# Optimization experiments

Hardware: AMD Instinct MI355X
Metric: run time of the kernel (lower is better)

## Reference

```python
import jax, jax.numpy as jnp
import numpy as np
from jax.scipy.special import logsumexp

NUM_TAGS = 128
B, S = 256, 1024


def setup_inputs() -> dict:
    key = jax.random.key(0)
    k1, k2, k3, k4, k5 = jax.random.split(key, 5)
    emissions = jax.random.normal(k1, (B, S, NUM_TAGS), dtype=jnp.float32)
    masks = jnp.ones((B, S), dtype=jnp.float32)
    tags = jax.random.randint(k2, (B, S), 0, NUM_TAGS, dtype=jnp.int64)
    transitions = jax.random.normal(k3, (NUM_TAGS, NUM_TAGS), dtype=jnp.float32)
    start_transitions = jax.random.normal(k4, (NUM_TAGS,), dtype=jnp.float32)
    end_transitions = jax.random.normal(k5, (NUM_TAGS,), dtype=jnp.float32)
    return {"emissions": emissions, "masks": masks, "tags": tags,
            "transitions": transitions, "start_transitions": start_transitions,
            "end_transitions": end_transitions}


def _crf_loss(emissions, masks, tags, transitions, start_transitions, end_transitions):
    b, s, t = emissions.shape

    # ---- forward algorithm (log partition) ----
    def step(alpha, xs):
        emit, m = xs  # emit: (B,T), m: (B,)
        # next[b,j] = logsumexp_i(alpha[b,i] + trans[i,j] + emit[b,j])
        nxt = logsumexp(alpha[:, :, None] + transitions[None, :, :] + emit[:, None, :], axis=1)
        alpha = jnp.where(m[:, None] > 0, nxt, alpha)
        return alpha, None

    alpha0 = jnp.broadcast_to(start_transitions[None, :], (b, t))
    # note: original torch code includes i=0 in the recurrence (applies transitions
    # from start_transitions into the first emission) -- replicated faithfully.
    alpha, _ = jax.lax.scan(step, alpha0,
                            (jnp.swapaxes(emissions, 0, 1), masks.T))
    log_z = logsumexp(alpha + end_transitions[None, :], axis=1)  # (B,)

    # ---- gold sequence score (vectorized over time) ----
    bidx = jnp.arange(b)
    score = start_transitions[tags[:, 0]]
    emit_g = jnp.take_along_axis(emissions, tags[:, :, None], axis=2)[..., 0]  # (B,S)
    score = score + jnp.sum(emit_g[:, : s - 1] * masks[:, : s - 1], axis=1)
    trans_g = transitions[tags[:, : s - 1], tags[:, 1:]]  # (B,S-1)
    score = score + jnp.sum(trans_g * masks[:, 1:], axis=1)
    last_ix = jnp.maximum(jnp.sum(masks, axis=1) - 1.0, 0.0).astype(jnp.int32)
    score = score + emissions[bidx, last_ix, tags[:, -1]] * masks[:, -1]
    score = score + end_transitions[tags[:, -1]] * masks[:, -1]

    return jnp.mean(log_z - score)


def reference(emissions, masks, tags, transitions, start_transitions, end_transitions):
    return _crf_loss(emissions, masks, tags, transitions, start_transitions, end_transitions)
```

## Files before the change

kernel.cpp:

```cpp
#include <hip/hip_runtime.h>

#define NT 128
#define SEQ 1024
#define NB 256

typedef _Float16 half2v __attribute__((ext_vector_type(2)));

#define DPP_MAX_STEP(x, ctrl)                                                   \
    fmaxf((x), __builtin_bit_cast(float, __builtin_amdgcn_update_dpp(           \
        __builtin_bit_cast(int, (x)), __builtin_bit_cast(int, (x)),             \
        (ctrl), 0xf, 0xf, false)))

__device__ __forceinline__ float wave_max_dpp(float x) {
    x = DPP_MAX_STEP(x, 0x111);
    x = DPP_MAX_STEP(x, 0x112);
    x = DPP_MAX_STEP(x, 0x114);
    x = DPP_MAX_STEP(x, 0x118);
    x = DPP_MAX_STEP(x, 0x142);
    x = DPP_MAX_STEP(x, 0x143);
    return __builtin_bit_cast(float, __builtin_amdgcn_readlane(
        __builtin_bit_cast(int, x), 63));
}

#define CRF_STEP(RC, RN, MC, DO_PRE, K)                                          \
    {                                                                            \
        float mcur = MC;                                                         \
        if (DO_PRE) {                                                            \
            RC = *(const float2*)(emp + (K) * NT);                               \
            MC = mpp[K];                                                         \
        }                                                                        \
        float A[4] = {0.f, 0.f, 0.f, 0.f};                                       \
        float B[4] = {0.f, 0.f, 0.f, 0.f};                                       \
        _Pragma("unroll")                                                        \
        for (int j = 0; j < 64; ++j) {                                           \
            half2v p = __builtin_bit_cast(half2v,                                \
                __builtin_amdgcn_readlane((int)pk, j));                          \
            A[j & 3] = __builtin_amdgcn_fdot2(p, E0[j], A[j & 3], false);        \
            B[j & 3] = __builtin_amdgcn_fdot2(p, E1[j], B[j & 3], false);        \
        }                                                                        \
        float v0 = ((A[0] + A[1]) + (A[2] + A[3])) * ex.x;                       \
        float v1 = ((B[0] + B[1]) + (B[2] + B[3])) * ex.y;                       \
        if (mcur > 0.0f) { cur0 = v0; cur1 = v1; offset += offadd; }             \
        pk = __builtin_bit_cast(unsigned int,                                    \
                                __builtin_amdgcn_cvt_pkrtz(cur0, cur1));         \
        mx  = wave_max_dpp(fmaxf(cur0, cur1));                                   \
        inv = __builtin_amdgcn_rcpf(256.0f * mx);                                \
        offadd = __logf(mx) + 5.545177444479562f;                                \
        ex.x = __expf(RN.x) * inv;                                               \
        ex.y = __expf(RN.y) * inv;                                               \
    }

__global__ __launch_bounds__(64, 1) void crf_scan_kernel(
    const float* __restrict__ emissions,
    const float* __restrict__ masks,
    const int*   __restrict__ tags,
    const float* __restrict__ transitions,
    const float* __restrict__ start_t,
    const float* __restrict__ end_t,
    float* __restrict__ out_per_batch)
{
    const int b  = blockIdx.x;
    const int l  = threadIdx.x;
    const int c0 = 2 * l;
    const int c1 = 2 * l + 1;

    __shared__ float msk_s[SEQ];

    half2v E0[64], E1[64];
    #pragma unroll
    for (int r = 0; r < 64; ++r) {
        float2 ta = *(const float2*)&transitions[(2 * r)     * NT + c0];
        float2 tb = *(const float2*)&transitions[(2 * r + 1) * NT + c0];
        E0[r] = half2v{(_Float16)__expf(ta.x), (_Float16)__expf(tb.x)};
        E1[r] = half2v{(_Float16)__expf(ta.y), (_Float16)__expf(tb.y)};
    }

    for (int s = l; s < SEQ; s += 64)
        msk_s[s] = masks[b * SEQ + s];

    float cur0 = __expf(start_t[c0]);
    float cur1 = __expf(start_t[c1]);
    unsigned int pk = __builtin_bit_cast(unsigned int,
                                        __builtin_amdgcn_cvt_pkrtz(cur0, cur1));
    float offset = 0.0f;

    float mx  = wave_max_dpp(fmaxf(cur0, cur1));
    float inv = __builtin_amdgcn_rcpf(256.0f * mx);
    float offadd = __logf(mx) + 5.545177444479562f;

    const float* eb  = emissions + (size_t)b * SEQ * NT;
    const float* mkp = masks + b * SEQ;

    float2 ring0 = *(const float2*)&eb[(size_t)0 * NT + c0];
    float2 ring1 = *(const float2*)&eb[(size_t)1 * NT + c0];
    float2 ring2 = *(const float2*)&eb[(size_t)2 * NT + c0];
    float2 ring3 = *(const float2*)&eb[(size_t)3 * NT + c0];
    float  mr0 = mkp[0], mr1 = mkp[1], mr2 = mkp[2], mr3 = mkp[3];

    float2 ex;
    ex.x = __expf(ring0.x) * inv;
    ex.y = __expf(ring0.y) * inv;

    const float* emp = eb + 4 * NT + c0;
    const float* mpp = mkp + 4;

    for (int it = 0; it < (SEQ - 4) / 4; ++it) {
        CRF_STEP(ring0, ring1, mr0, true, 0)
        CRF_STEP(ring1, ring2, mr1, true, 1)
        CRF_STEP(ring2, ring3, mr2, true, 2)
        CRF_STEP(ring3, ring0, mr3, true, 3)
        emp += 4 * NT;
        mpp += 4;
    }
    CRF_STEP(ring0, ring1, mr0, false, 0)
    CRF_STEP(ring1, ring2, mr1, false, 0)
    CRF_STEP(ring2, ring3, mr2, false, 0)
    CRF_STEP(ring3, ring3, mr3, false, 0)

    float term = cur0 * __expf(end_t[c0]) + cur1 * __expf(end_t[c1]);
    #pragma unroll
    for (int off = 32; off; off >>= 1)
        term += __shfl_xor(term, off);
    float log_z = offset + __logf(term);

    const int tb = b * SEQ;
    float sc = 0.0f, sm = 0.0f;
    for (int s = l; s < SEQ; s += 64) {
        float m = msk_s[s];
        sm += m;
        if (s < SEQ - 1) {
            int tg  = tags[tb + s];
            int tg1 = tags[tb + s + 1];
            sc += eb[(size_t)s * NT + tg] * m;
            sc += transitions[tg * NT + tg1] * msk_s[s + 1];
        }
    }
    #pragma unroll
    for (int off = 32; off; off >>= 1) {
        sc += __shfl_xor(sc, off);
        sm += __shfl_xor(sm, off);
    }

    if (l == 0) {
        int tg0 = tags[tb];
        int tgl = tags[tb + SEQ - 1];
        sc += start_t[tg0];
        int last_ix = (int)fmaxf(sm - 1.0f, 0.0f);
        float ml = msk_s[SEQ - 1];
        sc += eb[(size_t)last_ix * NT + tgl] * ml;
        sc += end_t[tgl] * ml;
        out_per_batch[b] = log_z - sc;
    }
}

__global__ void crf_reduce_kernel(const float* __restrict__ pb, float* __restrict__ out)
{
    float v = pb[threadIdx.x];
    #pragma unroll
    for (int off = 32; off; off >>= 1)
        v += __shfl_xor(v, off);
    __shared__ float s4[4];
    if ((threadIdx.x & 63) == 0) s4[threadIdx.x >> 6] = v;
    __syncthreads();
    if (threadIdx.x == 0)
        out[0] = (s4[0] + s4[1] + s4[2] + s4[3]) * (1.0f / 256.0f);
}

extern "C" void kernel_launch(void* const* d_in, const int* in_sizes, int n_in,
                              void* d_out, int out_size, void* d_ws, size_t ws_size,
                              hipStream_t stream) {
    const float* emissions   = (const float*)d_in[0];
    const float* masks       = (const float*)d_in[1];
    const int*   tags        = (const int*)  d_in[2];
    const float* transitions = (const float*)d_in[3];
    const float* start_t     = (const float*)d_in[4];
    const float* end_t       = (const float*)d_in[5];
    float* per_batch = (float*)d_ws;

    crf_scan_kernel<<<NB, 64, 0, stream>>>(emissions, masks, tags, transitions,
                                           start_t, end_t, per_batch);
    crf_reduce_kernel<<<1, 256, 0, stream>>>(per_batch, (float*)d_out);
}
```

Before: 678.6 us.

## Split CRF forward recurrence across four waves with LDS broadcast

Each batch row now uses 256 threads instead of one wave. Every lane owns one output tag and half of the source tags, and the two halves are combined with a cross-lane shuffle. The previous state is broadcast through a double-buffered LDS array instead of 64 readlanes per step, and the normalising max is reduced across waves through LDS. This cuts per-wave serial instruction count per time step, at the cost of a block-wide barrier and LDS round trip on every step of the recurrence.

```diff
diff --git a/kernel.cpp b/kernel.cpp
--- a/kernel.cpp
+++ b/kernel.cpp
@@ -22,35 +22,43 @@
         __builtin_bit_cast(int, x), 63));
 }
 
-#define CRF_STEP(RC, RN, MC, DO_PRE, K)                                          \
+#define CRF_STEP(RC, RN, MC, DO_PRE, K, BUF)                                     \
     {                                                                            \
         float mcur = MC;                                                         \
-        if (DO_PRE) {                                                            \
-            RC = *(const float2*)(emp + (K) * NT);                               \
-            MC = mpp[K];                                                         \
+        if (DO_PRE) { RC = emp[(K) * NT]; MC = mpp[K]; }                         \
+        const uint4* p4 = (const uint4*)&p_lds[BUF][ih * 32];                    \
+        float A0=0.f, A1=0.f, A2=0.f, A3=0.f;                                    \
+        _Pragma("unroll")                                                        \
+        for (int qi = 0; qi < 8; ++qi) {                                         \
+            uint4 q = p4[qi];                                                    \
+            A0 = __builtin_amdgcn_fdot2(__builtin_bit_cast(half2v, q.x),         \
+                                        E[4*qi+0], A0, false);                   \
+            A1 = __builtin_amdgcn_fdot2(__builtin_bit_cast(half2v, q.y),         \
+                                        E[4*qi+1], A1, false);                   \
+            A2 = __builtin_amdgcn_fdot2(__builtin_bit_cast(half2v, q.z),         \
+                                        E[4*qi+2], A2, false);                   \
+            A3 = __builtin_amdgcn_fdot2(__builtin_bit_cast(half2v, q.w),         \
+                                        E[4*qi+3], A3, false);                   \
         }                                                                        \
-        float A[4] = {0.f, 0.f, 0.f, 0.f};                                       \
-        float B[4] = {0.f, 0.f, 0.f, 0.f};                                       \
-        _Pragma("unroll")                                                        \
-        for (int j = 0; j < 64; ++j) {                                           \
-            half2v p = __builtin_bit_cast(half2v,                                \
-                __builtin_amdgcn_readlane((int)pk, j));                          \
-            A[j & 3] = __builtin_amdgcn_fdot2(p, E0[j], A[j & 3], false);        \
-            B[j & 3] = __builtin_amdgcn_fdot2(p, E1[j], B[j & 3], false);        \
-        }                                                                        \
-        float v0 = ((A[0] + A[1]) + (A[2] + A[3])) * ex.x;                       \
-        float v1 = ((B[0] + B[1]) + (B[2] + B[3])) * ex.y;                       \
-        if (mcur > 0.0f) { cur0 = v0; cur1 = v1; offset += offadd; }             \
-        pk = __builtin_bit_cast(unsigned int,                                    \
-                                __builtin_amdgcn_cvt_pkrtz(cur0, cur1));         \
-        mx  = wave_max_dpp(fmaxf(cur0, cur1));                                   \
+        float sv = (A0 + A1) + (A2 + A3);                                        \
+        sv += __shfl_xor(sv, 32);                  \
+        float v = sv * ex;                                                       \
+        if (mcur > 0.0f) { cur = v; offset += offadd; }                          \
+        float curo = __shfl_xor(cur, 1);        \
+        if (ih == 0 && (cl & 1) == 0)                                            \
+            p_lds[(BUF)^1][16*w + (cl >> 1)] = __builtin_bit_cast(unsigned int,  \
+                __builtin_amdgcn_cvt_pkrtz(cur, curo));                          \
+        float wm = wave_max_dpp(cur);                                            \
+        if (l == 0) wmax[(BUF)^1][w] = wm;                                       \
+        __syncthreads();                                                         \
+        float4 wv = *(const float4*)&wmax[(BUF)^1][0];                           \
+        mx = fmaxf(fmaxf(wv.x, wv.y), fmaxf(wv.z, wv.w));                        \
         inv = __builtin_amdgcn_rcpf(256.0f * mx);                                \
         offadd = __logf(mx) + 5.545177444479562f;                                \
-        ex.x = __expf(RN.x) * inv;                                               \
-        ex.y = __expf(RN.y) * inv;                                               \
-    }
-
-__global__ __launch_bounds__(64, 1) void crf_scan_kernel(
+        ex = __expf(RN) * inv;                                                   \
+    }
+
+__global__ __launch_bounds__(256, 1) void crf_scan_kernel(
     const float* __restrict__ emissions,
     const float* __restrict__ masks,
     const int*   __restrict__ tags,
@@ -59,78 +67,90 @@
     const float* __restrict__ end_t,
     float* __restrict__ out_per_batch)
 {
-    const int b  = blockIdx.x;
-    const int l  = threadIdx.x;
-    const int c0 = 2 * l;
-    const int c1 = 2 * l + 1;
-
+    const int b   = blockIdx.x;
+    const int tid = threadIdx.x;
+    const int w   = tid >> 6;
+    const int l   = tid & 63;
+    const int cl  = l & 31;
+    const int ih  = l >> 5;
+    const int c   = 32 * w + cl;
+    const int i0  = 64 * ih;
+
+    __shared__ __align__(16) unsigned int p_lds[2][64];
+    __shared__ __align__(16) float        wmax[2][4];
+    __shared__ float redA[4], redB[4], redC[4];
     __shared__ float msk_s[SEQ];
 
-    half2v E0[64], E1[64];
-    #pragma unroll
-    for (int r = 0; r < 64; ++r) {
-        float2 ta = *(const float2*)&transitions[(2 * r)     * NT + c0];
-        float2 tb = *(const float2*)&transitions[(2 * r + 1) * NT + c0];
-        E0[r] = half2v{(_Float16)__expf(ta.x), (_Float16)__expf(tb.x)};
-        E1[r] = half2v{(_Float16)__expf(ta.y), (_Float16)__expf(tb.y)};
-    }
-
-    for (int s = l; s < SEQ; s += 64)
+    half2v E[32];
+    #pragma unroll
+    for (int r = 0; r < 32; ++r) {
+        float ea = transitions[(i0 + 2*r    ) * NT + c];
+        float ob = transitions[(i0 + 2*r + 1) * NT + c];
+        E[r] = half2v{(_Float16)__expf(ea), (_Float16)__expf(ob)};
+    }
+
+    for (int s = tid; s < SEQ; s += 256)
         msk_s[s] = masks[b * SEQ + s];
 
-    float cur0 = __expf(start_t[c0]);
-    float cur1 = __expf(start_t[c1]);
-    unsigned int pk = __builtin_bit_cast(unsigned int,
-                                        __builtin_amdgcn_cvt_pkrtz(cur0, cur1));
+    float cur = __expf(start_t[c]);
     float offset = 0.0f;
 
-    float mx  = wave_max_dpp(fmaxf(cur0, cur1));
-    float inv = __builtin_amdgcn_rcpf(256.0f * mx);
+    {
+        float curo = __shfl_xor(cur, 1);
+        if (ih == 0 && (cl & 1) == 0)
+            p_lds[0][16*w + (cl >> 1)] = __builtin_bit_cast(unsigned int,
+                __builtin_amdgcn_cvt_pkrtz(cur, curo));
+        float wm = wave_max_dpp(cur);
+        if (l == 0) wmax[0][w] = wm;
+    }
+    __syncthreads();
+
+    float4 wv0 = *(const float4*)&wmax[0][0];
+    float mx   = fmaxf(fmaxf(wv0.x, wv0.y), fmaxf(wv0.z, wv0.w));
+    float inv  = __builtin_amdgcn_rcpf(256.0f * mx);
     float offadd = __logf(mx) + 5.545177444479562f;
 
     const float* eb  = emissions + (size_t)b * SEQ * NT;
     const float* mkp = masks + b * SEQ;
 
-    float2 ring0 = *(const float2*)&eb[(size_t)0 * NT + c0];
-    float2 ring1 = *(const float2*)&eb[(size_t)1 * NT + c0];
-    float2 ring2 = *(const float2*)&eb[(size_t)2 * NT + c0];
-    float2 ring3 = *(const float2*)&eb[(size_t)3 * NT + c0];
-    float  mr0 = mkp[0], mr1 = mkp[1], mr2 = mkp[2], mr3 = mkp[3];
-
-    float2 ex;
-    ex.x = __expf(ring0.x) * inv;
-    ex.y = __expf(ring0.y) * inv;
-
-    const float* emp = eb + 4 * NT + c0;
+    float ring0 = eb[(size_t)0 * NT + c];
+    float ring1 = eb[(size_t)1 * NT + c];
+    float ring2 = eb[(size_t)2 * NT + c];
+    float ring3 = eb[(size_t)3 * NT + c];
+    float mr0 = mkp[0], mr1 = mkp[1], mr2 = mkp[2], mr3 = mkp[3];
+
+    float ex = __expf(ring0) * inv;
+
+    const float* emp = eb + 4 * NT + c;
     const float* mpp = mkp + 4;
 
     for (int it = 0; it < (SEQ - 4) / 4; ++it) {
-        CRF_STEP(ring0, ring1, mr0, true, 0)
-        CRF_STEP(ring1, ring2, mr1, true, 1)
-        CRF_STEP(ring2, ring3, mr2, true, 2)
-        CRF_STEP(ring3, ring0, mr3, true, 3)
+        CRF_STEP(ring0, ring1, mr0, true, 0, 0)
+        CRF_STEP(ring1, ring2, mr1, true, 1, 1)
+        CRF_STEP(ring2, ring3, mr2, true, 2, 0)
+        CRF_STEP(ring3, ring0, mr3, true, 3, 1)
         emp += 4 * NT;
         mpp += 4;
     }
-    CRF_STEP(ring0, ring1, mr0, false, 0)
-    CRF_STEP(ring1, ring2, mr1, false, 0)
-    CRF_STEP(ring2, ring3, mr2, false, 0)
-    CRF_STEP(ring3, ring3, mr3, false, 0)
-
-    float term = cur0 * __expf(end_t[c0]) + cur1 * __expf(end_t[c1]);
+    CRF_STEP(ring0, ring1, mr0, false, 0, 0)
+    CRF_STEP(ring1, ring2, mr1, false, 0, 1)
+    CRF_STEP(ring2, ring3, mr2, false, 0, 0)
+    CRF_STEP(ring3, ring3, mr3, false, 0, 1)
+
+    float term = (ih == 0) ? cur * __expf(end_t[c]) : 0.0f;
     #pragma unroll
     for (int off = 32; off; off >>= 1)
         term += __shfl_xor(term, off);
-    float log_z = offset + __logf(term);
-
-    const int tb = b * SEQ;
+    if (l == 0) redA[w] = term;
+
+    const int tbase = b * SEQ;
     float sc = 0.0f, sm = 0.0f;
-    for (int s = l; s < SEQ; s += 64) {
+    for (int s = tid; s < SEQ; s += 256) {
         float m = msk_s[s];
         sm += m;
         if (s < SEQ - 1) {
-            int tg  = tags[tb + s];
-            int tg1 = tags[tb + s + 1];
+            int tg  = tags[tbase + s];
+            int tg1 = tags[tbase + s + 1];
             sc += eb[(size_t)s * NT + tg] * m;
             sc += transitions[tg * NT + tg1] * msk_s[s + 1];
         }
@@ -140,16 +160,22 @@
         sc += __shfl_xor(sc, off);
         sm += __shfl_xor(sm, off);
     }
-
-    if (l == 0) {
-        int tg0 = tags[tb];
-        int tgl = tags[tb + SEQ - 1];
-        sc += start_t[tg0];
-        int last_ix = (int)fmaxf(sm - 1.0f, 0.0f);
+    if (l == 0) { redB[w] = sc; redC[w] = sm; }
+    __syncthreads();
+
+    if (tid == 0) {
+        float term_t = (redA[0] + redA[1]) + (redA[2] + redA[3]);
+        float log_z  = offset + __logf(term_t);
+        float sct    = (redB[0] + redB[1]) + (redB[2] + redB[3]);
+        float smt    = (redC[0] + redC[1]) + (redC[2] + redC[3]);
+        int tg0 = tags[tbase];
+        int tgl = tags[tbase + SEQ - 1];
+        sct += start_t[tg0];
+        int last_ix = (int)fmaxf(smt - 1.0f, 0.0f);
         float ml = msk_s[SEQ - 1];
-        sc += eb[(size_t)last_ix * NT + tgl] * ml;
-        sc += end_t[tgl] * ml;
-        out_per_batch[b] = log_z - sc;
+        sct += eb[(size_t)last_ix * NT + tgl] * ml;
+        sct += end_t[tgl] * ml;
+        out_per_batch[b] = log_z - sct;
     }
 }
 
@@ -177,7 +203,7 @@
     const float* end_t       = (const float*)d_in[5];
     float* per_batch = (float*)d_ws;
 
-    crf_scan_kernel<<<NB, 64, 0, stream>>>(emissions, masks, tags, transitions,
-                                           start_t, end_t, per_batch);
+    crf_scan_kernel<<<NB, 256, 0, stream>>>(emissions, masks, tags, transitions,
+                                            start_t, end_t, per_batch);
     crf_reduce_kernel<<<1, 256, 0, stream>>>(per_batch, (float*)d_out);
 }
```

Result: faster. 646.2 us (-4.8%).

## Batch 16 sequences per block and compute CRF recurrence with MFMA

Applied to the files above, without the earlier changes.

Replaces the per-batch single-wave readlane/fdot2 recurrence with blocks of 4 waves, each handling 16 batch rows. Each step is a 16x128 by 128x128 matrix multiply done with f16 MFMA instructions; the probabilities are exchanged through double-buffered, swizzled LDS, and the per-row max is reduced across waves. This cuts the serial scalar dot-product work per step and shares the transition matrix across batches. In exchange it adds a block barrier every step and uses only 16 blocks, so occupancy is low and each step's latency depends on LDS round trips and the barrier.

```diff
diff --git a/kernel.cpp b/kernel.cpp
--- a/kernel.cpp
+++ b/kernel.cpp
@@ -3,54 +3,133 @@
 #define NT 128
 #define SEQ 1024
 #define NB 256
+#define NBLK 16
+#define BPB 16
 
 typedef _Float16 half2v __attribute__((ext_vector_type(2)));
+typedef _Float16 half8  __attribute__((ext_vector_type(8)));
+typedef float    f32x4  __attribute__((ext_vector_type(4)));
 
 #define DPP_MAX_STEP(x, ctrl)                                                   \
     fmaxf((x), __builtin_bit_cast(float, __builtin_amdgcn_update_dpp(           \
         __builtin_bit_cast(int, (x)), __builtin_bit_cast(int, (x)),             \
         (ctrl), 0xf, 0xf, false)))
-
-__device__ __forceinline__ float wave_max_dpp(float x) {
+#define DPP_ADD_STEP(x, ctrl)                                                   \
+    ((x) + __builtin_bit_cast(float, __builtin_amdgcn_update_dpp(               \
+        0, __builtin_bit_cast(int, (x)), (ctrl), 0xf, 0xf, true)))
+
+__device__ __forceinline__ float max16_dpp(float x) {
     x = DPP_MAX_STEP(x, 0x111);
     x = DPP_MAX_STEP(x, 0x112);
     x = DPP_MAX_STEP(x, 0x114);
     x = DPP_MAX_STEP(x, 0x118);
-    x = DPP_MAX_STEP(x, 0x142);
-    x = DPP_MAX_STEP(x, 0x143);
-    return __builtin_bit_cast(float, __builtin_amdgcn_readlane(
-        __builtin_bit_cast(int, x), 63));
-}
-
-#define CRF_STEP(RC, RN, MC, DO_PRE, K)                                          \
+    return x;
+}
+__device__ __forceinline__ float sum16_dpp(float x) {
+    x = DPP_ADD_STEP(x, 0x111);
+    x = DPP_ADD_STEP(x, 0x112);
+    x = DPP_ADD_STEP(x, 0x114);
+    x = DPP_ADD_STEP(x, 0x118);
+    return x;
+}
+__device__ __forceinline__ float swap1_dpp(float x) {
+    return __builtin_bit_cast(float, __builtin_amdgcn_update_dpp(
+        0, __builtin_bit_cast(int, x), 0xB1, 0xf, 0xf, true));
+}
+
+__device__ __forceinline__ void barrier_lds() {
+    asm volatile("s_waitcnt lgkmcnt(0)\n\ts_barrier" ::: "memory");
+}
+
+__device__ __forceinline__ f32x4 mfma16(uint4 a, uint4 b, f32x4 c) {
+    return __builtin_amdgcn_mfma_f32_16x16x32_f16(
+        __builtin_bit_cast(half8, a), __builtin_bit_cast(half8, b), c, 0, 0, 0);
+}
+
+#define BUILD_BF(dst, T, KC)                                                     \
     {                                                                            \
-        float mcur = MC;                                                         \
+        const int ct_ = 32*w + 16*(T) + li;                                      \
+        const int kb_ = (KC)*32 + lg*8;                                          \
+        half2v h0_, h1_, h2_, h3_;                                               \
+        h0_.x = (_Float16)__expf(transitions[(kb_+0)*NT + ct_]);                 \
+        h0_.y = (_Float16)__expf(transitions[(kb_+1)*NT + ct_]);                 \
+        h1_.x = (_Float16)__expf(transitions[(kb_+2)*NT + ct_]);                 \
+        h1_.y = (_Float16)__expf(transitions[(kb_+3)*NT + ct_]);                 \
+        h2_.x = (_Float16)__expf(transitions[(kb_+4)*NT + ct_]);                 \
+        h2_.y = (_Float16)__expf(transitions[(kb_+5)*NT + ct_]);                 \
+        h3_.x = (_Float16)__expf(transitions[(kb_+6)*NT + ct_]);                 \
+        h3_.y = (_Float16)__expf(transitions[(kb_+7)*NT + ct_]);                 \
+        dst.x = __builtin_bit_cast(unsigned int, h0_);                           \
+        dst.y = __builtin_bit_cast(unsigned int, h1_);                           \
+        dst.z = __builtin_bit_cast(unsigned int, h2_);                           \
+        dst.w = __builtin_bit_cast(unsigned int, h3_);                           \
+    }
+
+#define CRF_STEP(EMC, EMN, BUF, DO_PRE)                                          \
+    {                                                                            \
         if (DO_PRE) {                                                            \
-            RC = *(const float2*)(emp + (K) * NT);                               \
-            MC = mpp[K];                                                         \
+            _Pragma("unroll")                                                    \
+            for (int j = 0; j < 8; ++j) {                                        \
+                eoff[j] += NT;                                                   \
+                EMN[j] = emissions[eoff[j]];                                     \
+            }                                                                    \
         }                                                                        \
-        float A[4] = {0.f, 0.f, 0.f, 0.f};                                       \
-        float B[4] = {0.f, 0.f, 0.f, 0.f};                                       \
+        const uint2 mw_ = *(const uint2*)&msk16[scur][4 * lg];                   \
+        float xf_[8];                                                            \
         _Pragma("unroll")                                                        \
-        for (int j = 0; j < 64; ++j) {                                           \
-            half2v p = __builtin_bit_cast(half2v,                                \
-                __builtin_amdgcn_readlane((int)pk, j));                          \
-            A[j & 3] = __builtin_amdgcn_fdot2(p, E0[j], A[j & 3], false);        \
-            B[j & 3] = __builtin_amdgcn_fdot2(p, E1[j], B[j & 3], false);        \
+        for (int j = 0; j < 8; ++j) xf_[j] = __expf(EMC[j]);                     \
+        const uint4 af0 = *(const uint4*)&p_lds[BUF][abase + (( 0 + lg*4) ^ swzA)]; \
+        const uint4 af1 = *(const uint4*)&p_lds[BUF][abase + ((16 + lg*4) ^ swzA)]; \
+        const uint4 af2 = *(const uint4*)&p_lds[BUF][abase + ((32 + lg*4) ^ swzA)]; \
+        const uint4 af3 = *(const uint4*)&p_lds[BUF][abase + ((48 + lg*4) ^ swzA)]; \
+        f32x4 c0_ = {0.f, 0.f, 0.f, 0.f};                                        \
+        f32x4 c1_ = {0.f, 0.f, 0.f, 0.f};                                        \
+        c0_ = mfma16(af0, bf00, c0_);  c1_ = mfma16(af0, bf10, c1_);             \
+        c0_ = mfma16(af1, bf01, c0_);  c1_ = mfma16(af1, bf11, c1_);             \
+        c0_ = mfma16(af2, bf02, c0_);  c1_ = mfma16(af2, bf12, c1_);             \
+        c0_ = mfma16(af3, bf03, c0_);  c1_ = mfma16(af3, bf13, c1_);             \
+        const unsigned int mlo_ = mw_.x, mhi_ = mw_.y;                           \
+        _Pragma("unroll")                                                        \
+        for (int r_ = 0; r_ < 4; ++r_) {                                         \
+            const unsigned int mbits_ =                                          \
+                (r_ == 0) ? (mlo_ & 0xffffu) : (r_ == 1) ? (mlo_ >> 16)          \
+              : (r_ == 2) ? (mhi_ & 0xffffu) : (mhi_ >> 16);                     \
+            const float v0_ = c0_[r_] * xf_[r_]     * inv[r_];                   \
+            const float v1_ = c1_[r_] * xf_[4 + r_] * inv[r_];                   \
+            if (mbits_ != 0u) {                                                  \
+                cur0[r_] = v0_; cur1[r_] = v1_;                                  \
+                offset[r_] += offadd[r_];                                        \
+            }                                                                    \
         }                                                                        \
-        float v0 = ((A[0] + A[1]) + (A[2] + A[3])) * ex.x;                       \
-        float v1 = ((B[0] + B[1]) + (B[2] + B[3])) * ex.y;                       \
-        if (mcur > 0.0f) { cur0 = v0; cur1 = v1; offset += offadd; }             \
-        pk = __builtin_bit_cast(unsigned int,                                    \
-                                __builtin_amdgcn_cvt_pkrtz(cur0, cur1));         \
-        mx  = wave_max_dpp(fmaxf(cur0, cur1));                                   \
-        inv = __builtin_amdgcn_rcpf(256.0f * mx);                                \
-        offadd = __logf(mx) + 5.545177444479562f;                                \
-        ex.x = __expf(RN.x) * inv;                                               \
-        ex.y = __expf(RN.y) * inv;                                               \
-    }
-
-__global__ __launch_bounds__(64, 1) void crf_scan_kernel(
+        _Pragma("unroll")                                                        \
+        for (int r_ = 0; r_ < 4; ++r_) {                                         \
+            const float p0o_ = swap1_dpp(cur0[r_]);                              \
+            const float p1o_ = swap1_dpp(cur1[r_]);                              \
+            if ((li & 1) == 0) {                                                 \
+                const int b_ = 4 * lg + r_;                                      \
+                const unsigned int sw_ = (unsigned int)((b_ & 7) << 2);          \
+                p_lds[(BUF) ^ 1][b_*64 + ((unsigned int)kp0 ^ sw_)] =            \
+                    __builtin_bit_cast(unsigned int,                             \
+                        __builtin_amdgcn_cvt_pkrtz(cur0[r_], p0o_));             \
+                p_lds[(BUF) ^ 1][b_*64 + ((unsigned int)(kp0 + 8) ^ sw_)] =      \
+                    __builtin_bit_cast(unsigned int,                             \
+                        __builtin_amdgcn_cvt_pkrtz(cur1[r_], p1o_));             \
+            }                                                                    \
+            const float rm_ = max16_dpp(fmaxf(cur0[r_], cur1[r_]));              \
+            if (li == 15) wmax[(BUF) ^ 1][(4*lg + r_)*4 + w] = rm_;              \
+        }                                                                        \
+        barrier_lds();                                                           \
+        _Pragma("unroll")                                                        \
+        for (int r_ = 0; r_ < 4; ++r_) {                                         \
+            const float4 wv_ = *(const float4*)&wmax[(BUF) ^ 1][(4*lg + r_)*4];  \
+            const float mx_ = fmaxf(fmaxf(wv_.x, wv_.y), fmaxf(wv_.z, wv_.w));   \
+            inv[r_] = __builtin_amdgcn_rcpf(256.0f * mx_);                       \
+            offadd[r_] = __logf(mx_) + 5.545177444479562f;                       \
+        }                                                                        \
+        ++scur;                                                                  \
+    }
+
+__global__ __launch_bounds__(256, 1) void crf_scan_kernel(
     const float* __restrict__ emissions,
     const float* __restrict__ masks,
     const int*   __restrict__ tags,
@@ -59,97 +138,139 @@
     const float* __restrict__ end_t,
     float* __restrict__ out_per_batch)
 {
-    const int b  = blockIdx.x;
-    const int l  = threadIdx.x;
-    const int c0 = 2 * l;
-    const int c1 = 2 * l + 1;
-
-    __shared__ float msk_s[SEQ];
-
-    half2v E0[64], E1[64];
+    const int b16 = blockIdx.x * BPB;
+    const int tid = threadIdx.x;
+    const int w   = tid >> 6;
+    const int l   = tid & 63;
+    const int li  = l & 15;
+    const int lg  = l >> 4;
+
+    __shared__ __align__(16) unsigned int p_lds[2][16 * 64];
+    __shared__ __align__(16) float wmax[2][64];
+    __shared__ __align__(8)  _Float16 msk16[SEQ][BPB];
+    __shared__ __align__(16) float tsum_l[64];
+    __shared__ float off_l[16], sc_l[16], sm_l[16];
+
+    const int abase = li * 64;
+    const unsigned int swzA = (unsigned int)((li & 7) << 2);
+    const int kp0 = 16 * w + (li >> 1);
+
+    uint4 bf00, bf01, bf02, bf03, bf10, bf11, bf12, bf13;
+    BUILD_BF(bf00, 0, 0) BUILD_BF(bf01, 0, 1) BUILD_BF(bf02, 0, 2) BUILD_BF(bf03, 0, 3)
+    BUILD_BF(bf10, 1, 0) BUILD_BF(bf11, 1, 1) BUILD_BF(bf12, 1, 2) BUILD_BF(bf13, 1, 3)
+
+    {
+        const int bb = tid >> 4, s0 = tid & 15;
+        const float* mp = masks + (size_t)(b16 + bb) * SEQ;
+        for (int s = s0; s < SEQ; s += 16)
+            msk16[s][bb] = (_Float16)mp[s];
+    }
+
+    for (int u = tid; u < 16 * 64; u += 256) {
+        const int b_ = u & 15, kp_ = u >> 4;
+        const float e0 = __expf(start_t[2 * kp_]);
+        const float e1 = __expf(start_t[2 * kp_ + 1]);
+        p_lds[0][b_*64 + ((unsigned int)kp_ ^ (unsigned int)((b_ & 7) << 2))] =
+            __builtin_bit_cast(unsigned int, __builtin_amdgcn_cvt_pkrtz(e0, e1));
+    }
+
+    float cur0[4], cur1[4], offset[4], inv[4], offadd[4];
+    {
+        const float cs0 = __expf(start_t[32 * w + li]);
+        const float cs1 = __expf(start_t[32 * w + 16 + li]);
+        #pragma unroll
+        for (int r = 0; r < 4; ++r) {
+            cur0[r] = cs0; cur1[r] = cs1; offset[r] = 0.f;
+            const float rm = max16_dpp(fmaxf(cs0, cs1));
+            if (li == 15) wmax[0][(4*lg + r)*4 + w] = rm;
+        }
+    }
+
+    unsigned int eoff[8];
     #pragma unroll
-    for (int r = 0; r < 64; ++r) {
-        float2 ta = *(const float2*)&transitions[(2 * r)     * NT + c0];
-        float2 tb = *(const float2*)&transitions[(2 * r + 1) * NT + c0];
-        E0[r] = half2v{(_Float16)__expf(ta.x), (_Float16)__expf(tb.x)};
-        E1[r] = half2v{(_Float16)__expf(ta.y), (_Float16)__expf(tb.y)};
-    }
-
-    for (int s = l; s < SEQ; s += 64)
-        msk_s[s] = masks[b * SEQ + s];
-
-    float cur0 = __expf(start_t[c0]);
-    float cur1 = __expf(start_t[c1]);
-    unsigned int pk = __builtin_bit_cast(unsigned int,
-                                        __builtin_amdgcn_cvt_pkrtz(cur0, cur1));
-    float offset = 0.0f;
-
-    float mx  = wave_max_dpp(fmaxf(cur0, cur1));
-    float inv = __builtin_amdgcn_rcpf(256.0f * mx);
-    float offadd = __logf(mx) + 5.545177444479562f;
-
-    const float* eb  = emissions + (size_t)b * SEQ * NT;
-    const float* mkp = masks + b * SEQ;
-
-    float2 ring0 = *(const float2*)&eb[(size_t)0 * NT + c0];
-    float2 ring1 = *(const float2*)&eb[(size_t)1 * NT + c0];
-    float2 ring2 = *(const float2*)&eb[(size_t)2 * NT + c0];
-    float2 ring3 = *(const float2*)&eb[(size_t)3 * NT + c0];
-    float  mr0 = mkp[0], mr1 = mkp[1], mr2 = mkp[2], mr3 = mkp[3];
-
-    float2 ex;
-    ex.x = __expf(ring0.x) * inv;
-    ex.y = __expf(ring0.y) * inv;
-
-    const float* emp = eb + 4 * NT + c0;
-    const float* mpp = mkp + 4;
-
-    for (int it = 0; it < (SEQ - 4) / 4; ++it) {
-        CRF_STEP(ring0, ring1, mr0, true, 0)
-        CRF_STEP(ring1, ring2, mr1, true, 1)
-        CRF_STEP(ring2, ring3, mr2, true, 2)
-        CRF_STEP(ring3, ring0, mr3, true, 3)
-        emp += 4 * NT;
-        mpp += 4;
-    }
-    CRF_STEP(ring0, ring1, mr0, false, 0)
-    CRF_STEP(ring1, ring2, mr1, false, 0)
-    CRF_STEP(ring2, ring3, mr2, false, 0)
-    CRF_STEP(ring3, ring3, mr3, false, 0)
-
-    float term = cur0 * __expf(end_t[c0]) + cur1 * __expf(end_t[c1]);
+    for (int j = 0; j < 8; ++j) {
+        const int t_ = j >> 2, r_ = j & 3;
+        eoff[j] = (unsigned int)(((b16 + 4*lg + r_) * SEQ) * NT + 32*w + 16*t_ + li);
+    }
+
+    __syncthreads();
+
     #pragma unroll
-    for (int off = 32; off; off >>= 1)
-        term += __shfl_xor(term, off);
-    float log_z = offset + __logf(term);
-
-    const int tb = b * SEQ;
-    float sc = 0.0f, sm = 0.0f;
-    for (int s = l; s < SEQ; s += 64) {
-        float m = msk_s[s];
-        sm += m;
-        if (s < SEQ - 1) {
-            int tg  = tags[tb + s];
-            int tg1 = tags[tb + s + 1];
-            sc += eb[(size_t)s * NT + tg] * m;
-            sc += transitions[tg * NT + tg1] * msk_s[s + 1];
-        }
-    }
+    for (int r = 0; r < 4; ++r) {
+        const float4 wv = *(const float4*)&wmax[0][(4*lg + r)*4];
+        const float mx = fmaxf(fmaxf(wv.x, wv.y), fmaxf(wv.z, wv.w));
+        inv[r] = __builtin_amdgcn_rcpf(256.0f * mx);
+        offadd[r] = __logf(mx) + 5.545177444479562f;
+    }
+
+    float ema[8], emb[8];
     #pragma unroll
-    for (int off = 32; off; off >>= 1) {
-        sc += __shfl_xor(sc, off);
-        sm += __shfl_xor(sm, off);
-    }
-
-    if (l == 0) {
-        int tg0 = tags[tb];
-        int tgl = tags[tb + SEQ - 1];
+    for (int j = 0; j < 8; ++j) ema[j] = emissions[eoff[j]];
+
+    int scur = 0;
+    for (int it = 0; it < (SEQ - 2) / 2; ++it) {
+        CRF_STEP(ema, emb, 0, true)
+        CRF_STEP(emb, ema, 1, true)
+    }
+    CRF_STEP(ema, emb, 0, false)
+    CRF_STEP(emb, ema, 1, false)
+
+    {
+        const float ee0 = __expf(end_t[32 * w + li]);
+        const float ee1 = __expf(end_t[32 * w + 16 + li]);
+        #pragma unroll
+        for (int r = 0; r < 4; ++r) {
+            float ts = cur0[r] * ee0 + cur1[r] * ee1;
+            ts = sum16_dpp(ts);
+            if (li == 15) tsum_l[(4*lg + r)*4 + w] = ts;
+        }
+        if (w == 0 && li == 15) {
+            #pragma unroll
+            for (int r = 0; r < 4; ++r) off_l[4*lg + r] = offset[r];
+        }
+    }
+    __syncthreads();
+
+    {
+        const int bb = tid >> 4, sl = tid & 15;
+        const int gb = b16 + bb;
+        const float* ebb = emissions + (size_t)gb * SEQ * NT;
+        const int tb = gb * SEQ;
+        float sc = 0.f, sm = 0.f;
+        for (int s = sl; s < SEQ; s += 16) {
+            const float m = (float)msk16[s][bb];
+            sm += m;
+            if (s < SEQ - 1) {
+                const int tg  = tags[tb + s];
+                const int tg1 = tags[tb + s + 1];
+                sc += ebb[(size_t)s * NT + tg] * m;
+                sc += transitions[tg * NT + tg1] * (float)msk16[s + 1][bb];
+            }
+        }
+        #pragma unroll
+        for (int off = 8; off; off >>= 1) {
+            sc += __shfl_xor(sc, off);
+            sm += __shfl_xor(sm, off);
+        }
+        if (sl == 0) { sc_l[bb] = sc; sm_l[bb] = sm; }
+    }
+    __syncthreads();
+
+    if (tid < 16) {
+        const int r = tid;
+        const int gb = b16 + r;
+        const float4 tv = *(const float4*)&tsum_l[r * 4];
+        const float log_z = off_l[r] + __logf((tv.x + tv.y) + (tv.z + tv.w));
+        float sc = sc_l[r];
+        const float smt = sm_l[r];
+        const int tg0 = tags[gb * SEQ];
+        const int tgl = tags[gb * SEQ + SEQ - 1];
         sc += start_t[tg0];
-        int last_ix = (int)fmaxf(sm - 1.0f, 0.0f);
-        float ml = msk_s[SEQ - 1];
-        sc += eb[(size_t)last_ix * NT + tgl] * ml;
+        const int last_ix = (int)fmaxf(smt - 1.0f, 0.0f);
+        const float ml = (float)msk16[SEQ - 1][r];
+        sc += emissions[((size_t)gb * SEQ + last_ix) * NT + tgl] * ml;
         sc += end_t[tgl] * ml;
-        out_per_batch[b] = log_z - sc;
+        out_per_batch[gb] = log_z - sc;
     }
 }
 
@@ -177,7 +298,7 @@
     const float* end_t       = (const float*)d_in[5];
     float* per_batch = (float*)d_ws;
 
-    crf_scan_kernel<<<NB, 64, 0, stream>>>(emissions, masks, tags, transitions,
-                                           start_t, end_t, per_batch);
+    crf_scan_kernel<<<NBLK, 256, 0, stream>>>(emissions, masks, tags, transitions,
+                                              start_t, end_t, per_batch);
     crf_reduce_kernel<<<1, 256, 0, stream>>>(per_batch, (float*)d_out);
 }
```

Measured after the change: 1.255 ms. 85.0% more time.
